# Optimization experiments

Measured on AMD Instinct MI355X. Metric: run time of the kernel, lower is better.

The kernel has to match this reference:

```python
import jax, jax.numpy as jnp
import numpy as np

B, D, Q = 2048, 256, 65536
TEMP = 0.1

def _l2n(x):
    # torch F.normalize: x / max(||x||, eps)
    n = jnp.sqrt(jnp.sum(x * x, axis=1, keepdims=True))
    return x / jnp.maximum(n, 1e-12)

def setup_inputs() -> dict:
    key = jax.random.key(0)
    ks = jax.random.split(key, 5)
    h1 = jax.random.normal(ks[0], (B, D), jnp.float32)
    h2 = jax.random.normal(ks[1], (B, D), jnp.float32)
    W1 = jax.random.normal(ks[2], (D, D), jnp.float32) * (1.0 / np.sqrt(D))
    b1 = jnp.zeros((D,), jnp.float32)
    W2 = jax.random.normal(ks[3], (D, D), jnp.float32) * (1.0 / np.sqrt(D))
    b2 = jnp.zeros((D,), jnp.float32)
    fq = jax.random.normal(ks[4], (Q, D), jnp.float32)
    fq = _l2n(fq)  # queue is normalized at init in the torch module
    return {"h1": h1, "h2": h2, "W1": W1, "b1": b1, "W2": W2, "b2": b2, "feature_queue": fq}

def _project(h, W1, b1, W2, b2):
    return jnp.maximum(h @ W1 + b1, 0.0) @ W2 + b2

def _nearest_neighbor(zn, queue):
    # zn already L2-normalized [B, D]; queue [Q, D]
    sims = zn @ queue.T                     # [B, Q]
    idx = jnp.argmax(sims, axis=1)          # [B]
    nn_proj = queue[idx]                    # [B, D]
    # straight-through estimator
    return zn + jax.lax.stop_gradient(nn_proj - zn)

def _ce_diag(logits):
    # cross entropy with labels = arange(B)
    lsm = jax.nn.log_softmax(logits, axis=1)
    return -jnp.mean(jnp.diagonal(lsm))

def reference(h1, h2, W1, b1, W2, b2, feature_queue):
    z1 = _project(h1, W1, b1, W2, b2)
    z2 = _project(h2, W1, b1, W2, b2)
    z1n = _l2n(z1)
    z2n = _l2n(z2)
    nn_z1 = _nearest_neighbor(z1n, feature_queue)
    nn_z2 = _nearest_neighbor(z2n, feature_queue)
    loss = (_ce_diag(nn_z1 @ z2n.T / TEMP)
            + _ce_diag(z2n @ nn_z1.T / TEMP)
            + _ce_diag(nn_z2 @ z1n.T / TEMP)
            + _ce_diag(z1n @ nn_z2.T / TEMP)) / 4.0
    # FIFO queue update with detached normalized z1
    new_queue = jnp.concatenate([jax.lax.stop_gradient(z1n), feature_queue[:-B]], axis=0)
    return loss, new_queue
```

## Files before the change

kernel.cpp:

```cpp
#include <hip/hip_runtime.h>

typedef __bf16 bf16x8 __attribute__((ext_vector_type(8)));
typedef float f32x4 __attribute__((ext_vector_type(4)));
typedef unsigned short u16;
typedef unsigned long long u64;

static constexpr int D = 256;
static constexpr int BROWS = 2048;
static constexpr int QN = 65536;

__device__ __forceinline__ f32x4 mfma16(bf16x8 a, bf16x8 b, f32x4 c) {
  return __builtin_amdgcn_mfma_f32_16x16x32_bf16(a, b, c, 0, 0, 0);
}
__device__ __forceinline__ u16 bfb(float f) { return __builtin_bit_cast(u16, (__bf16)f); }

template<int ROWS>
__device__ __forceinline__ void stage_bf16(const u16* __restrict__ src, u16* lds, int tid) {
#pragma unroll
  for (int i = 0; i < ROWS / 8; ++i) {
    int slot = i * 256 + tid;
    int row = slot >> 5, s = slot & 31;
    bf16x8 d = *reinterpret_cast<const bf16x8*>(src + (size_t)row * D + s * 8);
    int byt = (row * 512 + s * 16) ^ ((row & 7) << 4);
    *reinterpret_cast<bf16x8*>(reinterpret_cast<char*>(lds) + byt) = d;
  }
}

template<int ROWS>
__device__ __forceinline__ void stage_f32(const float* __restrict__ src, u16* lds, int tid) {
#pragma unroll
  for (int i = 0; i < ROWS / 8; ++i) {
    int slot = i * 256 + tid;
    int row = slot >> 5, s = slot & 31;
    const float* p = src + (size_t)row * D + s * 8;
    float4 q0 = *reinterpret_cast<const float4*>(p);
    float4 q1 = *reinterpret_cast<const float4*>(p + 4);
    bf16x8 h;
    h[0] = (__bf16)q0.x; h[1] = (__bf16)q0.y; h[2] = (__bf16)q0.z; h[3] = (__bf16)q0.w;
    h[4] = (__bf16)q1.x; h[5] = (__bf16)q1.y; h[6] = (__bf16)q1.z; h[7] = (__bf16)q1.w;
    int byt = (row * 512 + s * 16) ^ ((row & 7) << 4);
    *reinterpret_cast<bf16x8*>(reinterpret_cast<char*>(lds) + byt) = h;
  }
}

__device__ __forceinline__ bf16x8 fragld(const u16* lds, int row, int ks, int lane) {
  int byt = (row * 512 + ((ks * 64 + ((lane >> 4) << 4)) ^ ((row & 7) << 4)));
  return *reinterpret_cast<const bf16x8*>(reinterpret_cast<const char*>(lds) + byt);
}

__global__ void wt_convert(const float* __restrict__ W1, const float* __restrict__ W2,
                           u16* __restrict__ Wt) {
  const float* W = blockIdx.x == 0 ? W1 : W2;
  u16* o = Wt + blockIdx.x * 65536;
  int n = threadIdx.x;
  int k0 = blockIdx.y * 32;
#pragma unroll
  for (int jj = 0; jj < 4; ++jj) {
    bf16x8 h;
#pragma unroll
    for (int j = 0; j < 8; ++j) h[j] = (__bf16)W[(size_t)(k0 + jj * 8 + j) * 256 + n];
    *reinterpret_cast<bf16x8*>(o + n * 256 + k0 + jj * 8) = h;
  }
}

template<bool SRC_F32, bool RELU>
__global__ __launch_bounds__(256) void proj_kernel(
    const float* __restrict__ h1, const float* __restrict__ h2,
    const u16* __restrict__ Asrc, const u16* __restrict__ Wt,
    const float* __restrict__ bias, u16* __restrict__ out_bf,
    float* __restrict__ out_f32) {
  __shared__ u16 Alds[64 * 256];
  __shared__ u16 Blds[128 * 256];
  int tid = threadIdx.x;
  int r0 = blockIdx.y * 64, n0 = blockIdx.x * 128;
  if constexpr (SRC_F32) {
    const float* src = (r0 < BROWS) ? (h1 + (size_t)r0 * D) : (h2 + (size_t)(r0 - BROWS) * D);
    stage_f32<64>(src, Alds, tid);
  } else {
    stage_bf16<64>(Asrc + (size_t)r0 * D, Alds, tid);
  }
  stage_bf16<128>(Wt + (size_t)n0 * D, Blds, tid);
  __syncthreads();

  int lane = tid & 63, w = tid >> 6, wm = w >> 1, wn = w & 1;
  f32x4 acc[2][4];
  const f32x4 vz = {0.f, 0.f, 0.f, 0.f};
#pragma unroll
  for (int m = 0; m < 2; ++m)
#pragma unroll
    for (int n = 0; n < 4; ++n) acc[m][n] = vz;

#pragma unroll
  for (int ks = 0; ks < 8; ++ks) {
    bf16x8 a[2], b[4];
#pragma unroll
    for (int i = 0; i < 2; ++i) a[i] = fragld(Alds, wm * 32 + i * 16 + (lane & 15), ks, lane);
#pragma unroll
    for (int i = 0; i < 4; ++i) b[i] = fragld(Blds, wn * 64 + i * 16 + (lane & 15), ks, lane);
#pragma unroll
    for (int m = 0; m < 2; ++m)
#pragma unroll
      for (int n = 0; n < 4; ++n) acc[m][n] = mfma16(a[m], b[n], acc[m][n]);
  }

#pragma unroll
  for (int m = 0; m < 2; ++m)
#pragma unroll
    for (int n = 0; n < 4; ++n)
#pragma unroll
      for (int j = 0; j < 4; ++j) {
        int row = r0 + wm * 32 + m * 16 + ((lane >> 4) << 2) + j;
        int col = n0 + wn * 64 + n * 16 + (lane & 15);
        float v = acc[m][n][j] + bias[col];
        if constexpr (RELU) {
          v = fmaxf(v, 0.f);
          out_bf[(size_t)row * D + col] = bfb(v);
        } else {
          out_f32[(size_t)row * D + col] = v;
        }
      }
}

__global__ void normalize_k(const float* __restrict__ Z, u16* __restrict__ ZNb,
                            float* __restrict__ outq) {
  int row = blockIdx.x * 4 + (threadIdx.x >> 6);
  int lane = threadIdx.x & 63;
  float4 v = *reinterpret_cast<const float4*>(Z + (size_t)row * D + lane * 4);
  float ss = v.x * v.x + v.y * v.y + v.z * v.z + v.w * v.w;
#pragma unroll
  for (int m = 1; m <= 32; m <<= 1) ss += __shfl_xor(ss, m, 64);
  float s = 1.f / fmaxf(sqrtf(ss), 1e-12f);
  float ox = v.x * s, oy = v.y * s, oz = v.z * s, ow = v.w * s;
  u64 pk = (u64)bfb(ox) | ((u64)bfb(oy) << 16) | ((u64)bfb(oz) << 32) | ((u64)bfb(ow) << 48);
  *reinterpret_cast<u64*>(ZNb + (size_t)row * D + lane * 4) = pk;
  if (row < BROWS) {
    float* p = outq + (size_t)row * D + lane * 4;
    p[0] = ox; p[1] = oy; p[2] = oz; p[3] = ow;
  }
}

__global__ __launch_bounds__(256, 2) void nn_gemm(const float* __restrict__ queue,
                                                  const u16* __restrict__ ZNb,
                                                  unsigned* __restrict__ nkey) {
  __shared__ char Abuf[2][32768];
  const int tid = threadIdx.x, lane = tid & 63, w = tid >> 6;
  const int bx = blockIdx.x, by = blockIdx.y;
  const int colbase = bx * 256 + w * 64;
  const int hi16 = (lane >> 4) << 4;

  bf16x8 b[4][8];
#pragma unroll
  for (int cf = 0; cf < 4; ++cf)
#pragma unroll
    for (int ks = 0; ks < 8; ++ks) {
      const float* p = queue + (size_t)(colbase + cf * 16 + (lane & 15)) * D + ks * 32 + ((lane >> 4) << 3);
      float4 q0 = *reinterpret_cast<const float4*>(p);
      float4 q1 = *reinterpret_cast<const float4*>(p + 4);
      bf16x8 h;
      h[0] = (__bf16)q0.x; h[1] = (__bf16)q0.y; h[2] = (__bf16)q0.z; h[3] = (__bf16)q0.w;
      h[4] = (__bf16)q1.x; h[5] = (__bf16)q1.y; h[6] = (__bf16)q1.z; h[7] = (__bf16)q1.w;
      b[cf][ks] = h;
    }

  int goff[8];
#pragma unroll
  for (int c = 0; c < 8; ++c) {
    int r = w * 16 + c * 2 + (lane >> 5);
    int s = lane & 31;
    goff[c] = r * 512 + ((s ^ (r & 7)) << 4);
  }

  const char* gbase = (const char*)ZNb + (size_t)by * 1048576;

#pragma unroll
  for (int c = 0; c < 8; ++c)
    __builtin_amdgcn_global_load_lds((const unsigned*)(gbase + goff[c]),
                                     (unsigned*)(Abuf[0] + w * 8192 + c * 1024), 16, 0, 0);

  const unsigned idbase = (unsigned)((lane >> 4) << 2);
  const int sw = (lane & 7) << 4;
  for (int i = 0; i < 32; ++i) {
    {
      const char* g = gbase + (size_t)((i + 1) & 31) * 32768;
      char* dst = Abuf[(i + 1) & 1] + w * 8192;
#pragma unroll
      for (int c = 0; c < 8; ++c)
        __builtin_amdgcn_global_load_lds((const unsigned*)(g + goff[c]),
                                         (unsigned*)(dst + c * 1024), 16, 0, 0);
    }
    if (i == 0) {
      asm volatile("s_waitcnt vmcnt(8)" ::: "memory");
    } else {
      asm volatile("s_waitcnt vmcnt(12)" ::: "memory");
    }
    __builtin_amdgcn_s_barrier();
    __builtin_amdgcn_sched_barrier(0);

    f32x4 acc[4][4];
    const f32x4 vinit = {4.f, 4.f, 4.f, 4.f};
#pragma unroll
    for (int cf = 0; cf < 4; ++cf)
#pragma unroll
      for (int af = 0; af < 4; ++af) acc[cf][af] = vinit;

    const char* buf = Abuf[i & 1];
    const char* pe0 = buf + (lane & 15) * 512 + (hi16 ^ sw);
    const char* po0 = buf + (lane & 15) * 512 + ((64 + hi16) ^ sw);
    __builtin_amdgcn_s_setprio(1);
#pragma unroll
    for (int k2 = 0; k2 < 4; ++k2) {
      bf16x8 ae[4], ao[4];
#pragma unroll
      for (int af = 0; af < 4; ++af) {
        ae[af] = *reinterpret_cast<const bf16x8*>(pe0 + af * 8192 + k2 * 128);
        ao[af] = *reinterpret_cast<const bf16x8*>(po0 + af * 8192 + k2 * 128);
      }
#pragma unroll
      for (int cf = 0; cf < 4; ++cf)
#pragma unroll
        for (int af = 0; af < 4; ++af)
          acc[cf][af] = mfma16(b[cf][2 * k2], ae[af], acc[cf][af]);
#pragma unroll
      for (int cf = 0; cf < 4; ++cf)
#pragma unroll
        for (int af = 0; af < 4; ++af)
          acc[cf][af] = mfma16(b[cf][2 * k2 + 1], ao[af], acc[cf][af]);
    }
    __builtin_amdgcn_s_setprio(0);

    const int chunk = by * 32 + i;
    unsigned kk[4];
#pragma unroll
    for (int af = 0; af < 4; ++af) {
      unsigned m01, m23;
      {
        unsigned c0 = (__float_as_uint(acc[0][af][0]) & 0xFFFFFFC0u) | (idbase + 0);
        unsigned c1 = (__float_as_uint(acc[0][af][1]) & 0xFFFFFFC0u) | (idbase + 1);
        unsigned c2 = (__float_as_uint(acc[0][af][2]) & 0xFFFFFFC0u) | (idbase + 2);
        unsigned c3 = (__float_as_uint(acc[0][af][3]) & 0xFFFFFFC0u) | (idbase + 3);
        unsigned d0 = (__float_as_uint(acc[1][af][0]) & 0xFFFFFFC0u) | (idbase + 16);
        unsigned d1 = (__float_as_uint(acc[1][af][1]) & 0xFFFFFFC0u) | (idbase + 17);
        unsigned d2 = (__float_as_uint(acc[1][af][2]) & 0xFFFFFFC0u) | (idbase + 18);
        unsigned d3 = (__float_as_uint(acc[1][af][3]) & 0xFFFFFFC0u) | (idbase + 19);
        unsigned a = c0 > c1 ? c0 : c1, bb = c2 > c3 ? c2 : c3;
        unsigned c = d0 > d1 ? d0 : d1, d = d2 > d3 ? d2 : d3;
        a = a > bb ? a : bb; c = c > d ? c : d;
        m01 = a > c ? a : c;
      }
      {
        unsigned c0 = (__float_as_uint(acc[2][af][0]) & 0xFFFFFFC0u) | (idbase + 32);
        unsigned c1 = (__float_as_uint(acc[2][af][1]) & 0xFFFFFFC0u) | (idbase + 33);
        unsigned c2 = (__float_as_uint(acc[2][af][2]) & 0xFFFFFFC0u) | (idbase + 34);
        unsigned c3 = (__float_as_uint(acc[2][af][3]) & 0xFFFFFFC0u) | (idbase + 35);
        unsigned d0 = (__float_as_uint(acc[3][af][0]) & 0xFFFFFFC0u) | (idbase + 48);
        unsigned d1 = (__float_as_uint(acc[3][af][1]) & 0xFFFFFFC0u) | (idbase + 49);
        unsigned d2 = (__float_as_uint(acc[3][af][2]) & 0xFFFFFFC0u) | (idbase + 50);
        unsigned d3 = (__float_as_uint(acc[3][af][3]) & 0xFFFFFFC0u) | (idbase + 51);
        unsigned a = c0 > c1 ? c0 : c1, bb = c2 > c3 ? c2 : c3;
        unsigned c = d0 > d1 ? d0 : d1, d = d2 > d3 ? d2 : d3;
        a = a > bb ? a : bb; c = c > d ? c : d;
        m23 = a > c ? a : c;
      }
      unsigned k = m01 > m23 ? m01 : m23;
      unsigned o = (unsigned)__shfl_xor((int)k, 16, 64); if (o > k) k = o;
      o = (unsigned)__shfl_xor((int)k, 32, 64); if (o > k) k = o;
      kk[af] = k;
    }
    if (lane < 16) {
      size_t row0 = (size_t)(chunk * 64 + lane);
      nkey[row0 * 1024 + (bx << 2) + w] = kk[0];
      nkey[(row0 + 16) * 1024 + (bx << 2) + w] = kk[1];
      nkey[(row0 + 32) * 1024 + (bx << 2) + w] = kk[2];
      nkey[(row0 + 48) * 1024 + (bx << 2) + w] = kk[3];
    }

    __builtin_amdgcn_sched_barrier(0);
    __builtin_amdgcn_s_barrier();
  }
}

__global__ void nn_finish(const unsigned* __restrict__ nkey, const float* __restrict__ queue,
                          u16* __restrict__ NNb) {
  int row = blockIdx.x * 4 + (threadIdx.x >> 6);
  int lane = threadIdx.x & 63;
  const uint4* p = reinterpret_cast<const uint4*>(nkey + (size_t)row * 1024);
  uint4 q0 = p[lane], q1 = p[lane + 64], q2 = p[lane + 128], q3 = p[lane + 192];
  unsigned vs[16] = {q0.x, q0.y, q0.z, q0.w, q1.x, q1.y, q1.z, q1.w,
                     q2.x, q2.y, q2.z, q2.w, q3.x, q3.y, q3.z, q3.w};
  unsigned mx = 0;
#pragma unroll
  for (int t = 0; t < 16; ++t) mx = vs[t] > mx ? vs[t] : mx;
#pragma unroll
  for (int m = 1; m <= 32; m <<= 1) {
    unsigned o = (unsigned)__shfl_xor((int)mx, m, 64);
    if (o > mx) mx = o;
  }
  unsigned pos = 0xFFFFFFFFu;
#pragma unroll
  for (int t = 0; t < 16; ++t) {
    unsigned pp = (unsigned)((lane + (t >> 2) * 64) * 4 + (t & 3));
    if (vs[t] == mx && pp < pos) pos = pp;
  }
#pragma unroll
  for (int m = 1; m <= 32; m <<= 1) {
    unsigned o = (unsigned)__shfl_xor((int)pos, m, 64);
    if (o < pos) pos = o;
  }
  int idx = (int)(pos * 64 + (mx & 63u));
  float4 v = *(reinterpret_cast<const float4*>(queue + (size_t)idx * D) + lane);
  u64 pk = (u64)bfb(v.x) | ((u64)bfb(v.y) << 16) | ((u64)bfb(v.z) << 32) | ((u64)bfb(v.w) << 48);
  *reinterpret_cast<u64*>(NNb + (size_t)row * D + lane * 4) = pk;
}

__global__ __launch_bounds__(256) void ce_gemm(const u16* __restrict__ NNb,
                                               const u16* __restrict__ ZNb,
                                               float2* __restrict__ rowpart,
                                               float2* __restrict__ colpart,
                                               float* __restrict__ diag,
                                               const float* __restrict__ cq,
                                               float* __restrict__ copydst) {
  __shared__ u16 Alds[128 * 256];
  __shared__ u16 Blds[128 * 256];
  int tid = threadIdx.x;
  int cb = blockIdx.x, rb = blockIdx.y, mat = blockIdx.z;
  const u16* A = NNb + (size_t)(mat * BROWS + rb * 128) * D;
  const u16* Bm = ZNb + (size_t)((mat == 0 ? BROWS : 0) + cb * 128) * D;
  stage_bf16<128>(A, Alds, tid);
  stage_bf16<128>(Bm, Blds, tid);
  __syncthreads();

  int lane = tid & 63, w = tid >> 6, wm = w >> 1, wn = w & 1;
  f32x4 acc[4][4];
  const f32x4 vz = {0.f, 0.f, 0.f, 0.f};
#pragma unroll
  for (int m = 0; m < 4; ++m)
#pragma unroll
    for (int n = 0; n < 4; ++n) acc[m][n] = vz;

#pragma unroll
  for (int ks = 0; ks < 8; ++ks) {
    bf16x8 a[4], b[4];
#pragma unroll
    for (int i = 0; i < 4; ++i) a[i] = fragld(Alds, wm * 64 + i * 16 + (lane & 15), ks, lane);
#pragma unroll
    for (int i = 0; i < 4; ++i) b[i] = fragld(Blds, wn * 64 + i * 16 + (lane & 15), ks, lane);
#pragma unroll
    for (int m = 0; m < 4; ++m)
#pragma unroll
      for (int n = 0; n < 4; ++n) acc[m][n] = mfma16(a[m], b[n], acc[m][n]);
  }

#pragma unroll
  for (int m = 0; m < 4; ++m)
#pragma unroll
    for (int n = 0; n < 4; ++n) acc[m][n] = acc[m][n] * 10.f;

  int rbase = rb * 128 + wm * 64;
  int cbase = cb * 128 + wn * 64;

#pragma unroll
  for (int m = 0; m < 4; ++m)
#pragma unroll
    for (int j = 0; j < 4; ++j) {
      float mx = -3e38f;
#pragma unroll
      for (int n = 0; n < 4; ++n) mx = fmaxf(mx, acc[m][n][j]);
#pragma unroll
      for (int s = 1; s <= 8; s <<= 1) mx = fmaxf(mx, __shfl_xor(mx, s, 64));
      float sm = 0.f;
#pragma unroll
      for (int n = 0; n < 4; ++n) sm += __expf(acc[m][n][j] - mx);
#pragma unroll
      for (int s = 1; s <= 8; s <<= 1) sm += __shfl_xor(sm, s, 64);
      if ((lane & 15) == 0) {
        int r = rbase + m * 16 + ((lane >> 4) << 2) + j;
        rowpart[(((size_t)mat * BROWS + r) << 5) + cb * 2 + wn] = make_float2(mx, sm);
      }
    }

#pragma unroll
  for (int n = 0; n < 4; ++n) {
    float mx = -3e38f;
#pragma unroll
    for (int m = 0; m < 4; ++m)
#pragma unroll
      for (int j = 0; j < 4; ++j) mx = fmaxf(mx, acc[m][n][j]);
#pragma unroll
    for (int s = 16; s <= 32; s <<= 1) mx = fmaxf(mx, __shfl_xor(mx, s, 64));
    float sm = 0.f;
#pragma unroll
    for (int m = 0; m < 4; ++m)
#pragma unroll
      for (int j = 0; j < 4; ++j) sm += __expf(acc[m][n][j] - mx);
#pragma unroll
    for (int s = 16; s <= 32; s <<= 1) sm += __shfl_xor(sm, s, 64);
    if (lane < 16) {
      int c = cbase + n * 16 + lane;
      colpart[(((size_t)mat * BROWS + c) << 5) + rb * 2 + wm] = make_float2(mx, sm);
    }
  }

#pragma unroll
  for (int m = 0; m < 4; ++m)
#pragma unroll
    for (int n = 0; n < 4; ++n)
#pragma unroll
      for (int j = 0; j < 4; ++j) {
        int rg = rbase + m * 16 + ((lane >> 4) << 2) + j;
        int cg = cbase + n * 16 + (lane & 15);
        if (rg == cg) diag[mat * BROWS + rg] = acc[m][n][j];
      }

  {
    int cbid = cb + rb * 16 + mat * 256;
    const float4* src = reinterpret_cast<const float4*>(cq);
    float4* dst = reinterpret_cast<float4*>(copydst);
    size_t base = (size_t)cbid * 7936 + (size_t)tid;
#pragma unroll 4
    for (int k = 0; k < 31; ++k) dst[base + (size_t)k * 256] = src[base + (size_t)k * 256];
  }
}

__global__ void loss_part(const float2* __restrict__ rowpart, const float2* __restrict__ colpart,
                          const float* __restrict__ diag, float* __restrict__ lpart) {
  __shared__ float red[256];
  int tid = threadIdx.x;
  int r = blockIdx.x * 64 + (tid >> 2), q = tid & 3;
  const float2* rp = rowpart + ((size_t)r << 5) + q * 8;
  float2 e[8];
#pragma unroll
  for (int i = 0; i < 8; ++i) e[i] = rp[i];
  float mx = e[0].x;
#pragma unroll
  for (int i = 1; i < 8; ++i) mx = fmaxf(mx, e[i].x);
  mx = fmaxf(mx, __shfl_xor(mx, 1, 64));
  mx = fmaxf(mx, __shfl_xor(mx, 2, 64));
  float s = 0.f;
#pragma unroll
  for (int i = 0; i < 8; ++i) s += e[i].y * __expf(e[i].x - mx);
  s += __shfl_xor(s, 1, 64);
  s += __shfl_xor(s, 2, 64);
  float rlse = mx + __logf(s);

  const float2* cp = colpart + ((size_t)r << 5) + q * 8;
#pragma unroll
  for (int i = 0; i < 8; ++i) e[i] = cp[i];
  float mx2 = e[0].x;
#pragma unroll
  for (int i = 1; i < 8; ++i) mx2 = fmaxf(mx2, e[i].x);
  mx2 = fmaxf(mx2, __shfl_xor(mx2, 1, 64));
  mx2 = fmaxf(mx2, __shfl_xor(mx2, 2, 64));
  float s2 = 0.f;
#pragma unroll
  for (int i = 0; i < 8; ++i) s2 += e[i].y * __expf(e[i].x - mx2);
  s2 += __shfl_xor(s2, 1, 64);
  s2 += __shfl_xor(s2, 2, 64);
  float clse = mx2 + __logf(s2);

  red[tid] = (q == 0) ? (rlse + clse - 2.f * diag[r]) : 0.f;
  __syncthreads();
  for (int st = 128; st > 0; st >>= 1) {
    if (tid < st) red[tid] += red[tid + st];
    __syncthreads();
  }
  if (tid == 0) lpart[blockIdx.x] = red[0];
}

__global__ void loss_final(const float* __restrict__ lpart, float* __restrict__ out) {
  int lane = threadIdx.x;
  float v = lpart[lane];
#pragma unroll
  for (int m = 1; m <= 32; m <<= 1) v += __shfl_xor(v, m, 64);
  if (lane == 0) out[0] = v * (1.f / 8192.f);
}

extern "C" void kernel_launch(void* const* d_in, const int* in_sizes, int n_in,
                              void* d_out, int out_size, void* d_ws, size_t ws_size,
                              hipStream_t stream) {
  const float* h1 = (const float*)d_in[0];
  const float* h2 = (const float*)d_in[1];
  const float* W1 = (const float*)d_in[2];
  const float* b1 = (const float*)d_in[3];
  const float* W2 = (const float*)d_in[4];
  const float* b2 = (const float*)d_in[5];
  const float* fq = (const float*)d_in[6];
  float* out = (float*)d_out;

  char* ws = (char*)d_ws;
  u16* Wt        = (u16*)(ws);
  u16* Ybf       = (u16*)(ws + 262144);
  float* Z       = (float*)(ws + 2359296);
  u16* ZNb       = (u16*)(ws + 6553600);
  unsigned* nkey = (unsigned*)(ws + 8650752);
  u16* NNb       = (u16*)(ws + 25444352);
  float2* rowp   = (float2*)(ws + 27541504);
  float2* colp   = (float2*)(ws + 28590080);
  float* diag    = (float*)(ws + 29638656);
  float* lpart   = (float*)(ws + 29655040);

  wt_convert<<<dim3(2, 8), dim3(256), 0, stream>>>(W1, W2, Wt);
  proj_kernel<true, true><<<dim3(2, 64), dim3(256), 0, stream>>>(
      h1, h2, (const u16*)nullptr, Wt, b1, Ybf, (float*)nullptr);
  proj_kernel<false, false><<<dim3(2, 64), dim3(256), 0, stream>>>(
      (const float*)nullptr, (const float*)nullptr, Ybf, Wt + 65536, b2, (u16*)nullptr, Z);
  normalize_k<<<dim3(1024), dim3(256), 0, stream>>>(Z, ZNb, out + 1);
  nn_gemm<<<dim3(256, 2), dim3(256), 0, stream>>>(fq, ZNb, nkey);
  nn_finish<<<dim3(1024), dim3(256), 0, stream>>>(nkey, fq, NNb);
  ce_gemm<<<dim3(16, 16, 2), dim3(256), 0, stream>>>(NNb, ZNb, rowp, colp, diag,
                                                     fq, out + 1 + (size_t)BROWS * D);
  loss_part<<<dim3(64), dim3(256), 0, stream>>>(rowp, colp, diag, lpart);
  loss_final<<<dim3(1), dim3(64), 0, stream>>>(lpart, out);
}
```

Before: 184.1 us.

## Split nn_gemm into single-wave blocks to remove workgroup barriers

Result: slower. 210.2 us (+14.2%).

```diff
diff --git a/kernel.cpp b/kernel.cpp
--- a/kernel.cpp
+++ b/kernel.cpp
@@ -139,13 +139,13 @@
   }
 }
 
-__global__ __launch_bounds__(256, 2) void nn_gemm(const float* __restrict__ queue,
-                                                  const u16* __restrict__ ZNb,
-                                                  unsigned* __restrict__ nkey) {
-  __shared__ char Abuf[2][32768];
-  const int tid = threadIdx.x, lane = tid & 63, w = tid >> 6;
+__global__ __launch_bounds__(64, 2) void nn_gemm(const float* __restrict__ queue,
+                                                 const u16* __restrict__ ZNb,
+                                                 unsigned* __restrict__ nkey) {
+  __shared__ char Abuf[2][8192];
+  const int lane = threadIdx.x;
   const int bx = blockIdx.x, by = blockIdx.y;
-  const int colbase = bx * 256 + w * 64;
+  const int colbase = bx * 64;
   const int hi16 = (lane >> 4) << 4;
 
   bf16x8 b[4][8];
@@ -165,97 +165,83 @@
   int goff[8];
 #pragma unroll
   for (int c = 0; c < 8; ++c) {
-    int r = w * 16 + c * 2 + (lane >> 5);
+    int r = c * 2 + (lane >> 5);
     int s = lane & 31;
     goff[c] = r * 512 + ((s ^ (r & 7)) << 4);
   }
 
-  const char* gbase = (const char*)ZNb + (size_t)by * 1048576;
+  const char* gbase = (const char*)ZNb + (size_t)(by * 2048) * 512;
 
 #pragma unroll
   for (int c = 0; c < 8; ++c)
     __builtin_amdgcn_global_load_lds((const unsigned*)(gbase + goff[c]),
-                                     (unsigned*)(Abuf[0] + w * 8192 + c * 1024), 16, 0, 0);
+                                     (unsigned*)(Abuf[0] + c * 1024), 16, 0, 0);
 
   const unsigned idbase = (unsigned)((lane >> 4) << 2);
   const int sw = (lane & 7) << 4;
-  for (int i = 0; i < 32; ++i) {
+  for (int i = 0; i < 128; ++i) {
+    if (i == 0) {
+      asm volatile("s_waitcnt vmcnt(0)" ::: "memory");
+    } else {
+      asm volatile("s_waitcnt vmcnt(1)" ::: "memory");
+    }
+    __builtin_amdgcn_sched_barrier(0);
+
+    f32x4 acc[4];
+    const f32x4 vinit = {4.f, 4.f, 4.f, 4.f};
+#pragma unroll
+    for (int cf = 0; cf < 4; ++cf) acc[cf] = vinit;
+
+    const char* buf = Abuf[i & 1];
+    const char* pe = buf + (lane & 15) * 512 + (hi16 ^ sw);
+    const char* po = buf + (lane & 15) * 512 + ((64 + hi16) ^ sw);
+    __builtin_amdgcn_s_setprio(1);
+#pragma unroll
+    for (int k2 = 0; k2 < 4; ++k2) {
+      bf16x8 a_e = *reinterpret_cast<const bf16x8*>(pe + k2 * 128);
+      bf16x8 a_o = *reinterpret_cast<const bf16x8*>(po + k2 * 128);
+#pragma unroll
+      for (int cf = 0; cf < 4; ++cf) acc[cf] = mfma16(b[cf][2 * k2], a_e, acc[cf]);
+#pragma unroll
+      for (int cf = 0; cf < 4; ++cf) acc[cf] = mfma16(b[cf][2 * k2 + 1], a_o, acc[cf]);
+    }
+    __builtin_amdgcn_s_setprio(0);
+
     {
-      const char* g = gbase + (size_t)((i + 1) & 31) * 32768;
-      char* dst = Abuf[(i + 1) & 1] + w * 8192;
+      const char* g = gbase + (size_t)((i + 1) & 127) * 8192;
+      char* dst = Abuf[(i + 1) & 1];
 #pragma unroll
       for (int c = 0; c < 8; ++c)
         __builtin_amdgcn_global_load_lds((const unsigned*)(g + goff[c]),
                                          (unsigned*)(dst + c * 1024), 16, 0, 0);
     }
-    if (i == 0) {
-      asm volatile("s_waitcnt vmcnt(8)" ::: "memory");
-    } else {
-      asm volatile("s_waitcnt vmcnt(12)" ::: "memory");
-    }
-    __builtin_amdgcn_s_barrier();
-    __builtin_amdgcn_sched_barrier(0);
-
-    f32x4 acc[4][4];
-    const f32x4 vinit = {4.f, 4.f, 4.f, 4.f};
-#pragma unroll
-    for (int cf = 0; cf < 4; ++cf)
-#pragma unroll
-      for (int af = 0; af < 4; ++af) acc[cf][af] = vinit;
-
-    const char* buf = Abuf[i & 1];
-    const char* pe0 = buf + (lane & 15) * 512 + (hi16 ^ sw);
-    const char* po0 = buf + (lane & 15) * 512 + ((64 + hi16) ^ sw);
-    __builtin_amdgcn_s_setprio(1);
-#pragma unroll
-    for (int k2 = 0; k2 < 4; ++k2) {
-      bf16x8 ae[4], ao[4];
-#pragma unroll
-      for (int af = 0; af < 4; ++af) {
-        ae[af] = *reinterpret_cast<const bf16x8*>(pe0 + af * 8192 + k2 * 128);
-        ao[af] = *reinterpret_cast<const bf16x8*>(po0 + af * 8192 + k2 * 128);
-      }
-#pragma unroll
-      for (int cf = 0; cf < 4; ++cf)
-#pragma unroll
-        for (int af = 0; af < 4; ++af)
-          acc[cf][af] = mfma16(b[cf][2 * k2], ae[af], acc[cf][af]);
-#pragma unroll
-      for (int cf = 0; cf < 4; ++cf)
-#pragma unroll
-        for (int af = 0; af < 4; ++af)
-          acc[cf][af] = mfma16(b[cf][2 * k2 + 1], ao[af], acc[cf][af]);
-    }
-    __builtin_amdgcn_s_setprio(0);
-
-    const int chunk = by * 32 + i;
-    unsigned kk[4];
-#pragma unroll
-    for (int af = 0; af < 4; ++af) {
+
+    unsigned kk;
+    {
       unsigned m01, m23;
       {
-        unsigned c0 = (__float_as_uint(acc[0][af][0]) & 0xFFFFFFC0u) | (idbase + 0);
-        unsigned c1 = (__float_as_uint(acc[0][af][1]) & 0xFFFFFFC0u) | (idbase + 1);
-        unsigned c2 = (__float_as_uint(acc[0][af][2]) & 0xFFFFFFC0u) | (idbase + 2);
-        unsigned c3 = (__float_as_uint(acc[0][af][3]) & 0xFFFFFFC0u) | (idbase + 3);
-        unsigned d0 = (__float_as_uint(acc[1][af][0]) & 0xFFFFFFC0u) | (idbase + 16);
-        unsigned d1 = (__float_as_uint(acc[1][af][1]) & 0xFFFFFFC0u) | (idbase + 17);
-        unsigned d2 = (__float_as_uint(acc[1][af][2]) & 0xFFFFFFC0u) | (idbase + 18);
-        unsigned d3 = (__float_as_uint(acc[1][af][3]) & 0xFFFFFFC0u) | (idbase + 19);
+        unsigned c0 = (__float_as_uint(acc[0][0]) & 0xFFFFFFC0u) | (idbase + 0);
+        unsigned c1 = (__float_as_uint(acc[0][1]) & 0xFFFFFFC0u) | (idbase + 1);
+        unsigned c2 = (__float_as_uint(acc[0][2]) & 0xFFFFFFC0u) | (idbase + 2);
+        unsigned c3 = (__float_as_uint(acc[0][3]) & 0xFFFFFFC0u) | (idbase + 3);
+        unsigned d0 = (__float_as_uint(acc[1][0]) & 0xFFFFFFC0u) | (idbase + 16);
+        unsigned d1 = (__float_as_uint(acc[1][1]) & 0xFFFFFFC0u) | (idbase + 17);
+        unsigned d2 = (__float_as_uint(acc[1][2]) & 0xFFFFFFC0u) | (idbase + 18);
+        unsigned d3 = (__float_as_uint(acc[1][3]) & 0xFFFFFFC0u) | (idbase + 19);
         unsigned a = c0 > c1 ? c0 : c1, bb = c2 > c3 ? c2 : c3;
         unsigned c = d0 > d1 ? d0 : d1, d = d2 > d3 ? d2 : d3;
         a = a > bb ? a : bb; c = c > d ? c : d;
         m01 = a > c ? a : c;
       }
       {
-        unsigned c0 = (__float_as_uint(acc[2][af][0]) & 0xFFFFFFC0u) | (idbase + 32);
-        unsigned c1 = (__float_as_uint(acc[2][af][1]) & 0xFFFFFFC0u) | (idbase + 33);
-        unsigned c2 = (__float_as_uint(acc[2][af][2]) & 0xFFFFFFC0u) | (idbase + 34);
-        unsigned c3 = (__float_as_uint(acc[2][af][3]) & 0xFFFFFFC0u) | (idbase + 35);
-        unsigned d0 = (__float_as_uint(acc[3][af][0]) & 0xFFFFFFC0u) | (idbase + 48);
-        unsigned d1 = (__float_as_uint(acc[3][af][1]) & 0xFFFFFFC0u) | (idbase + 49);
-        unsigned d2 = (__float_as_uint(acc[3][af][2]) & 0xFFFFFFC0u) | (idbase + 50);
-        unsigned d3 = (__float_as_uint(acc[3][af][3]) & 0xFFFFFFC0u) | (idbase + 51);
+        unsigned c0 = (__float_as_uint(acc[2][0]) & 0xFFFFFFC0u) | (idbase + 32);
+        unsigned c1 = (__float_as_uint(acc[2][1]) & 0xFFFFFFC0u) | (idbase + 33);
+        unsigned c2 = (__float_as_uint(acc[2][2]) & 0xFFFFFFC0u) | (idbase + 34);
+        unsigned c3 = (__float_as_uint(acc[2][3]) & 0xFFFFFFC0u) | (idbase + 35);
+        unsigned d0 = (__float_as_uint(acc[3][0]) & 0xFFFFFFC0u) | (idbase + 48);
+        unsigned d1 = (__float_as_uint(acc[3][1]) & 0xFFFFFFC0u) | (idbase + 49);
+        unsigned d2 = (__float_as_uint(acc[3][2]) & 0xFFFFFFC0u) | (idbase + 50);
+        unsigned d3 = (__float_as_uint(acc[3][3]) & 0xFFFFFFC0u) | (idbase + 51);
         unsigned a = c0 > c1 ? c0 : c1, bb = c2 > c3 ? c2 : c3;
         unsigned c = d0 > d1 ? d0 : d1, d = d2 > d3 ? d2 : d3;
         a = a > bb ? a : bb; c = c > d ? c : d;
@@ -264,18 +250,12 @@
       unsigned k = m01 > m23 ? m01 : m23;
       unsigned o = (unsigned)__shfl_xor((int)k, 16, 64); if (o > k) k = o;
       o = (unsigned)__shfl_xor((int)k, 32, 64); if (o > k) k = o;
-      kk[af] = k;
+      kk = k;
     }
     if (lane < 16) {
-      size_t row0 = (size_t)(chunk * 64 + lane);
-      nkey[row0 * 1024 + (bx << 2) + w] = kk[0];
-      nkey[(row0 + 16) * 1024 + (bx << 2) + w] = kk[1];
-      nkey[(row0 + 32) * 1024 + (bx << 2) + w] = kk[2];
-      nkey[(row0 + 48) * 1024 + (bx << 2) + w] = kk[3];
-    }
-
-    __builtin_amdgcn_sched_barrier(0);
-    __builtin_amdgcn_s_barrier();
+      size_t row0 = (size_t)(by * 2048 + i * 16 + lane);
+      nkey[row0 * 1024 + bx] = kk;
+    }
   }
 }
 
@@ -504,7 +484,7 @@
   proj_kernel<false, false><<<dim3(2, 64), dim3(256), 0, stream>>>(
       (const float*)nullptr, (const float*)nullptr, Ybf, Wt + 65536, b2, (u16*)nullptr, Z);
   normalize_k<<<dim3(1024), dim3(256), 0, stream>>>(Z, ZNb, out + 1);
-  nn_gemm<<<dim3(256, 2), dim3(256), 0, stream>>>(fq, ZNb, nkey);
+  nn_gemm<<<dim3(1024, 2), dim3(64), 0, stream>>>(fq, ZNb, nkey);
   nn_finish<<<dim3(1024), dim3(256), 0, stream>>>(nkey, fq, NNb);
   ce_gemm<<<dim3(16, 16, 2), dim3(256), 0, stream>>>(NNb, ZNb, rowp, colp, diag,
                                                      fq, out + 1 + (size_t)BROWS * D);
```
